# Performance work log

Hardware: AMD Instinct MI355X
Metric: run time of the kernel (lower is better)

Reference implementation:

```python
import jax, jax.numpy as jnp
import numpy as np

N = 100000
E = 1600000
IN_DIM = 128
HID = 64
NUM_CLASSES = 40
K = 3


def setup_inputs() -> dict:
    key = jax.random.key(0)
    ks = jax.random.split(key, 8)
    x = jax.random.normal(ks[0], (N, IN_DIM), dtype=jnp.float32)
    edge_index = jax.random.randint(ks[1], (2, E), 0, N, dtype=jnp.int32)
    s_in = 1.0 / np.sqrt(IN_DIM)
    s_h = 1.0 / np.sqrt(HID)
    W_in = jax.random.uniform(ks[2], (IN_DIM, HID), jnp.float32, -s_in, s_in)
    b_in = jax.random.uniform(ks[3], (HID,), jnp.float32, -s_in, s_in)
    W_layers = jax.random.uniform(ks[4], (K, HID, HID), jnp.float32, -s_h, s_h)
    b_layers = jax.random.uniform(ks[5], (K, HID), jnp.float32, -s_h, s_h)
    W_cls = jax.random.uniform(ks[6], (HID, NUM_CLASSES), jnp.float32, -s_h, s_h)
    b_cls = jax.random.uniform(ks[7], (NUM_CLASSES,), jnp.float32, -s_h, s_h)
    return {"x": x, "edge_index": edge_index, "W_in": W_in, "b_in": b_in,
            "W_layers": W_layers, "b_layers": b_layers, "W_cls": W_cls, "b_cls": b_cls}


def reference(x, edge_index, W_in, b_in, W_layers, b_layers, W_cls, b_cls):
    # eval mode: dropout is identity
    src, dst = edge_index[0], edge_index[1]
    h = jax.nn.relu(x @ W_in + b_in)  # [N, HID]
    for i in range(K):
        # gather messages from src nodes, scatter-add into dst nodes
        agg = jax.ops.segment_sum(h[src], dst, num_segments=N)  # [N, HID]
        h = jax.nn.relu((h + agg) @ W_layers[i] + b_layers[i])
    return h @ W_cls + b_cls  # [N, NUM_CLASSES]
```

## Files before the change

kernel.cpp:

```cpp
#include <hip/hip_runtime.h>
#include <hip/hip_bf16.h>

#define N_NODES 100000
#define E_NUM   1600000
#define IN_DIM  128
#define HID     64
#define NCLS    40
#define NBUCK   782
#define TILE_E  8192
#define NTILE   196
#define BCAP    3072
#define ZROW    N_NODES
#define NTILES_M 6250
#define IN_BLOCKS 1563

typedef __attribute__((ext_vector_type(8))) short bf16x8;
typedef __attribute__((ext_vector_type(4))) float f32x4;

static __device__ __forceinline__ float bflo(unsigned u) {
    return __uint_as_float(u << 16);
}
static __device__ __forceinline__ float bfhi(unsigned u) {
    return __uint_as_float(u & 0xFFFF0000u);
}
static __device__ __forceinline__ unsigned short f2bf(float f) {
    unsigned u = __float_as_uint(f);
    u += 0x7FFFu + ((u >> 16) & 1u);
    return (unsigned short)(u >> 16);
}
static __device__ __forceinline__ unsigned pack2bf(float lo, float hi) {
    return (unsigned)f2bf(lo) | ((unsigned)f2bf(hi) << 16);
}

__global__ void k_prep(const float* __restrict__ Win, const float* __restrict__ Wl,
                       const float* __restrict__ Wc, unsigned* __restrict__ pWin,
                       unsigned* __restrict__ pWl, unsigned* __restrict__ pWc,
                       int* __restrict__ cursor, unsigned short* __restrict__ H0,
                       unsigned short* __restrict__ H1)
{
    const int t = threadIdx.x;
    if (blockIdx.x == 0) {
        for (int i = t; i < NBUCK; i += 256) cursor[i] = 0;
        if (t < 32) {
            ((unsigned*)(H0 + (size_t)ZROW * HID))[t] = 0;
            ((unsigned*)(H1 + (size_t)ZROW * HID))[t] = 0;
        }
    }
    int i = blockIdx.x * 256 + t;
    if (i < 4096) {
        const int nt = i >> 10, ks = (i >> 8) & 3, ln = (i >> 2) & 63, jp = i & 3;
        const int n = nt * 16 + (ln & 15);
        const int k = ks * 32 + (ln >> 4) * 8 + jp * 2;
        pWin[i] = pack2bf(Win[k * HID + n], Win[(k + 1) * HID + n]);
    } else if (i < 10240) {
        int j = i - 4096;
        const int l = j >> 11; j &= 2047;
        const int nt = j >> 9, ks = (j >> 8) & 1, ln = (j >> 2) & 63, jp = j & 3;
        const int n = nt * 16 + (ln & 15);
        const int k = ks * 32 + (ln >> 4) * 8 + jp * 2;
        const float* w = Wl + (size_t)l * HID * HID;
        pWl[i - 4096] = pack2bf(w[k * HID + n], w[(k + 1) * HID + n]);
    } else if (i < 11776) {
        const int j = i - 10240;
        const int nt = j >> 9, ks = (j >> 8) & 1, ln = (j >> 2) & 63, jp = j & 3;
        const int n = nt * 16 + (ln & 15);
        const int k = ks * 32 + (ln >> 4) * 8 + jp * 2;
        pWc[j] = (n < NCLS) ? pack2bf(Wc[k * NCLS + n], Wc[(k + 1) * NCLS + n]) : 0u;
    }
}

__global__ __launch_bounds__(256) void k_build_ingemm(
    const int* __restrict__ ei, int* __restrict__ cursor, int* __restrict__ pairs,
    const float* __restrict__ x, const unsigned* __restrict__ pWin,
    const float* __restrict__ b, unsigned short* __restrict__ H0)
{
    __shared__ int lh[NBUCK];
    __shared__ int lbase[NBUCK];
    __shared__ int lcnt[NBUCK];
    const int t = threadIdx.x;

    if (blockIdx.x < NTILE) {
        for (int i = t; i < NBUCK; i += 256) { lh[i] = 0; lcnt[i] = 0; }
        __syncthreads();
        const int e0 = blockIdx.x * TILE_E;
        for (int k = 0; k < TILE_E; k += 256) {
            int e = e0 + k + t;
            if (e < E_NUM) atomicAdd(&lh[ei[E_NUM + e] >> 7], 1);
        }
        __syncthreads();
        for (int i = t; i < NBUCK; i += 256)
            lbase[i] = lh[i] ? atomicAdd(&cursor[i], lh[i]) : 0;
        __syncthreads();
        for (int k = 0; k < TILE_E; k += 256) {
            int e = e0 + k + t;
            if (e < E_NUM) {
                int src = ei[e];
                int dst = ei[E_NUM + e];
                int bkt = dst >> 7;
                int r   = lbase[bkt] + atomicAdd(&lcnt[bkt], 1);
                if (r < BCAP) pairs[bkt * BCAP + r] = (src << 7) | (dst & 127);
            }
        }
        return;
    }

    const int blk  = blockIdx.x - NTILE;
    const int lane = t & 63;
    const int w    = t >> 6;
    const int tile = blk * 4 + w;
    if (tile >= NTILES_M) return;
    const int quad = lane >> 4;
    const int mrow = lane & 15;
    const int gr   = tile * 16 + mrow;
    const float* xr = x + (size_t)gr * IN_DIM;
    const bf16x8* pb = (const bf16x8*)pWin;

    f32x4 acc0 = {0.f, 0.f, 0.f, 0.f};
    f32x4 acc1 = {0.f, 0.f, 0.f, 0.f};
    f32x4 acc2 = {0.f, 0.f, 0.f, 0.f};
    f32x4 acc3 = {0.f, 0.f, 0.f, 0.f};
    #pragma unroll
    for (int ks = 0; ks < 4; ++ks) {
        const float4 v0 = *(const float4*)(xr + ks * 32 + quad * 8);
        const float4 v1 = *(const float4*)(xr + ks * 32 + quad * 8 + 4);
        union { unsigned u[4]; bf16x8 v; } au;
        au.u[0] = pack2bf(v0.x, v0.y);
        au.u[1] = pack2bf(v0.z, v0.w);
        au.u[2] = pack2bf(v1.x, v1.y);
        au.u[3] = pack2bf(v1.z, v1.w);
        acc0 = __builtin_amdgcn_mfma_f32_16x16x32_bf16(au.v, pb[       ks * 64 + lane], acc0, 0, 0, 0);
        acc1 = __builtin_amdgcn_mfma_f32_16x16x32_bf16(au.v, pb[256 +  ks * 64 + lane], acc1, 0, 0, 0);
        acc2 = __builtin_amdgcn_mfma_f32_16x16x32_bf16(au.v, pb[512 +  ks * 64 + lane], acc2, 0, 0, 0);
        acc3 = __builtin_amdgcn_mfma_f32_16x16x32_bf16(au.v, pb[768 +  ks * 64 + lane], acc3, 0, 0, 0);
    }

    const int colg = lane & 15;
    const int nodeb = tile * 16 + quad * 4;
    const float bv0 = b[     colg];
    const float bv1 = b[16 + colg];
    const float bv2 = b[32 + colg];
    const float bv3 = b[48 + colg];
    #pragma unroll
    for (int r = 0; r < 4; ++r) {
        const size_t ob = (size_t)(nodeb + r) * HID;
        H0[ob      + colg] = f2bf(fmaxf(acc0[r] + bv0, 0.f));
        H0[ob + 16 + colg] = f2bf(fmaxf(acc1[r] + bv1, 0.f));
        H0[ob + 32 + colg] = f2bf(fmaxf(acc2[r] + bv2, 0.f));
        H0[ob + 48 + colg] = f2bf(fmaxf(acc3[r] + bv3, 0.f));
    }
}

__global__ __launch_bounds__(256) void k_bsort(
    const int* __restrict__ cursor, const int* __restrict__ pairs,
    int* __restrict__ srcs, int* __restrict__ row_start, int* __restrict__ row_end)
{
    __shared__ int cnt[128];
    __shared__ int sc[128];
    __shared__ int cur[128];
    const int t = threadIdx.x;
    const int b = blockIdx.x;
    const int beg = b * BCAP;
    const int n_e = min(cursor[b], BCAP);
    if (t < 128) cnt[t] = 0;
    __syncthreads();
    for (int i = t; i < n_e; i += 256)
        atomicAdd(&cnt[pairs[beg + i] & 127], 1);
    __syncthreads();
    if (t < 128) sc[t] = (cnt[t] + 7) & ~7;
    __syncthreads();
    for (int off = 1; off < 128; off <<= 1) {
        int a = (t < 128 && t >= off) ? sc[t - off] : 0;
        __syncthreads();
        if (t < 128) sc[t] += a;
        __syncthreads();
    }
    const int node0 = b << 7;
    if (t < 128) {
        const int pc = (cnt[t] + 7) & ~7;
        const int ex = sc[t] - pc;
        cur[t] = ex;
        const int node = node0 + t;
        if (node < N_NODES) {
            const int rs = beg + ex;
            row_start[node] = rs;
            row_end  [node] = min(rs + pc, beg + BCAP);
        }
        const int fb = beg + ex + cnt[t];
        const int fe = min(beg + ex + pc, beg + BCAP);
        for (int i = fb; i < fe; ++i) srcs[i] = ZROW;
    }
    __syncthreads();
    for (int i = t; i < n_e; i += 256) {
        int p = pairs[beg + i];
        int r = atomicAdd(&cur[p & 127], 1);
        if (r < BCAP) srcs[beg + r] = p >> 7;
    }
}

static __device__ __forceinline__ void gather_tile(
    const int* __restrict__ row_start, const int* __restrict__ row_end,
    const int* __restrict__ srcs, const unsigned short* __restrict__ Hin,
    unsigned (*sup)[36], int row0, int t)
{
    const int lane = t & 63;
    const int w    = t >> 6;
    const int nd   = lane >> 4;
    const int sub  = (lane >> 3) & 1;
    const int fl   = lane & 7;
    const int node = row0 + (w << 2) + nd;

    const int rs = row_start[node];
    int rem = row_end[node] - rs;
    int i = rs + sub;

    float a0 = 0.f, a1 = 0.f, a2 = 0.f, a3 = 0.f;
    float a4 = 0.f, a5 = 0.f, a6 = 0.f, a7 = 0.f;

#define ACC8(u) do { \
        a0 += bflo((u).x); a1 += bfhi((u).x); \
        a2 += bflo((u).y); a3 += bfhi((u).y); \
        a4 += bflo((u).z); a5 += bfhi((u).z); \
        a6 += bflo((u).w); a7 += bfhi((u).w); } while (0)

    while (rem >= 16) {
        const int s0 = srcs[i     ], s1 = srcs[i +  2];
        const int s2 = srcs[i +  4], s3 = srcs[i +  6];
        const int s4 = srcs[i +  8], s5 = srcs[i + 10];
        const int s6 = srcs[i + 12], s7 = srcs[i + 14];
        const uint4 u0 = *(const uint4*)(Hin + (size_t)s0 * HID + 8 * fl);
        const uint4 u1 = *(const uint4*)(Hin + (size_t)s1 * HID + 8 * fl);
        const uint4 u2 = *(const uint4*)(Hin + (size_t)s2 * HID + 8 * fl);
        const uint4 u3 = *(const uint4*)(Hin + (size_t)s3 * HID + 8 * fl);
        const uint4 u4 = *(const uint4*)(Hin + (size_t)s4 * HID + 8 * fl);
        const uint4 u5 = *(const uint4*)(Hin + (size_t)s5 * HID + 8 * fl);
        const uint4 u6 = *(const uint4*)(Hin + (size_t)s6 * HID + 8 * fl);
        const uint4 u7 = *(const uint4*)(Hin + (size_t)s7 * HID + 8 * fl);
        ACC8(u0); ACC8(u1); ACC8(u2); ACC8(u3);
        ACC8(u4); ACC8(u5); ACC8(u6); ACC8(u7);
        i += 16; rem -= 16;
    }
    if (rem >= 8) {
        const int s0 = srcs[i    ], s1 = srcs[i + 2];
        const int s2 = srcs[i + 4], s3 = srcs[i + 6];
        const uint4 u0 = *(const uint4*)(Hin + (size_t)s0 * HID + 8 * fl);
        const uint4 u1 = *(const uint4*)(Hin + (size_t)s1 * HID + 8 * fl);
        const uint4 u2 = *(const uint4*)(Hin + (size_t)s2 * HID + 8 * fl);
        const uint4 u3 = *(const uint4*)(Hin + (size_t)s3 * HID + 8 * fl);
        ACC8(u0); ACC8(u1); ACC8(u2); ACC8(u3);
    }

    a0 += __shfl_xor(a0, 8, 64); a1 += __shfl_xor(a1, 8, 64);
    a2 += __shfl_xor(a2, 8, 64); a3 += __shfl_xor(a3, 8, 64);
    a4 += __shfl_xor(a4, 8, 64); a5 += __shfl_xor(a5, 8, 64);
    a6 += __shfl_xor(a6, 8, 64); a7 += __shfl_xor(a7, 8, 64);

    const uint4 us = *(const uint4*)(Hin + (size_t)node * HID + 8 * fl);
    ACC8(us);
#undef ACC8

    const int r = (w << 2) + nd;
    if (sub == 0) {
        sup[r][4 * fl    ] = pack2bf(a0, a1);
        sup[r][4 * fl + 1] = pack2bf(a2, a3);
    } else {
        sup[r][4 * fl + 2] = pack2bf(a4, a5);
        sup[r][4 * fl + 3] = pack2bf(a6, a7);
    }
}

__global__ __launch_bounds__(256) void k_gather_gemm(
    const int* __restrict__ row_start, const int* __restrict__ row_end,
    const int* __restrict__ srcs,
    const unsigned short* __restrict__ Hin, const unsigned* __restrict__ pWl,
    const float* __restrict__ bl, unsigned short* __restrict__ Hout)
{
    __shared__ unsigned sup[16][36];
    const int t = threadIdx.x;
    const int row0 = blockIdx.x * 16;
    gather_tile(row_start, row_end, srcs, Hin, sup, row0, t);
    __syncthreads();

    const int lane = t & 63;
    const int w    = t >> 6;
    const int quad = lane >> 4;
    const int m    = lane & 15;
    const bf16x8* pb = (const bf16x8*)pWl;
    f32x4 acc = {0.f, 0.f, 0.f, 0.f};
    #pragma unroll
    for (int ks = 0; ks < 2; ++ks) {
        const bf16x8 a  = *(const bf16x8*)&sup[m][ks * 16 + quad * 4];
        const bf16x8 bb = pb[((w << 1) + ks) * 64 + lane];
        acc = __builtin_amdgcn_mfma_f32_16x16x32_bf16(a, bb, acc, 0, 0, 0);
    }
    const int jc = w * 16 + m;
    const float bv = bl[jc];
    #pragma unroll
    for (int r = 0; r < 4; ++r) {
        const int node = row0 + quad * 4 + r;
        Hout[(size_t)node * HID + jc] = f2bf(fmaxf(acc[r] + bv, 0.f));
    }
}

__global__ __launch_bounds__(256) void k_gather_gemm_cls(
    const int* __restrict__ row_start, const int* __restrict__ row_end,
    const int* __restrict__ srcs,
    const unsigned short* __restrict__ Hin, const unsigned* __restrict__ pWl,
    const float* __restrict__ bl, const unsigned* __restrict__ pWc,
    const float* __restrict__ bc, float* __restrict__ out)
{
    __shared__ unsigned sup[16][36];
    __shared__ unsigned short sh2[16][72];
    const int t = threadIdx.x;
    const int row0 = blockIdx.x * 16;
    gather_tile(row_start, row_end, srcs, Hin, sup, row0, t);
    __syncthreads();

    const int lane = t & 63;
    const int w    = t >> 6;
    const int quad = lane >> 4;
    const int m    = lane & 15;
    const bf16x8* pb = (const bf16x8*)pWl;
    f32x4 acc = {0.f, 0.f, 0.f, 0.f};
    #pragma unroll
    for (int ks = 0; ks < 2; ++ks) {
        const bf16x8 a  = *(const bf16x8*)&sup[m][ks * 16 + quad * 4];
        const bf16x8 bb = pb[((w << 1) + ks) * 64 + lane];
        acc = __builtin_amdgcn_mfma_f32_16x16x32_bf16(a, bb, acc, 0, 0, 0);
    }
    const int jc = w * 16 + m;
    const float bv = bl[jc];
    #pragma unroll
    for (int r = 0; r < 4; ++r)
        sh2[quad * 4 + r][jc] = f2bf(fmaxf(acc[r] + bv, 0.f));
    __syncthreads();

    if (w < 3) {
        const bf16x8* pbc = (const bf16x8*)pWc;
        f32x4 c = {0.f, 0.f, 0.f, 0.f};
        #pragma unroll
        for (int ks = 0; ks < 2; ++ks) {
            const bf16x8 a = *(const bf16x8*)&sh2[m][ks * 32 + quad * 8];
            c = __builtin_amdgcn_mfma_f32_16x16x32_bf16(a, pbc[(w * 2 + ks) * 64 + lane], c, 0, 0, 0);
        }
        const int col = w * 16 + m;
        if (col < NCLS) {
            const float bcv = bc[col];
            #pragma unroll
            for (int r = 0; r < 4; ++r)
                out[(size_t)(row0 + quad * 4 + r) * NCLS + col] = c[r] + bcv;
        }
    }
}

extern "C" void kernel_launch(void* const* d_in, const int* in_sizes, int n_in,
                              void* d_out, int out_size, void* d_ws, size_t ws_size,
                              hipStream_t stream)
{
    const float* x        = (const float*)d_in[0];
    const int*   ei       = (const int*)  d_in[1];
    const float* W_in     = (const float*)d_in[2];
    const float* b_in     = (const float*)d_in[3];
    const float* W_layers = (const float*)d_in[4];
    const float* b_layers = (const float*)d_in[5];
    const float* W_cls    = (const float*)d_in[6];
    const float* b_cls    = (const float*)d_in[7];
    float* out = (float*)d_out;

    unsigned short* H0 = (unsigned short*)d_ws;
    unsigned short* H1 = H0 + (size_t)(N_NODES + 1) * HID;
    int* wsp       = (int*)(H1 + (size_t)(N_NODES + 1) * HID);
    int* pairs     = wsp;
    int* srcs      = wsp + NBUCK * BCAP;
    int* row_start = wsp + 2 * NBUCK * BCAP;
    int* row_end   = row_start + 100096;
    int* cursor    = row_end + 100096;
    unsigned* pWin = (unsigned*)(cursor + 1024);
    unsigned* pWl  = pWin + 4096;
    unsigned* pWc  = pWl + 6144;

    const int gemm_blocks = N_NODES / 16;

    k_prep        <<<46, 256, 0, stream>>>(W_in, W_layers, W_cls, pWin, pWl, pWc,
                                           cursor, H0, H1);
    k_build_ingemm<<<NTILE + IN_BLOCKS, 256, 0, stream>>>(ei, cursor, pairs,
                                                          x, pWin, b_in, H0);
    k_bsort       <<<NBUCK, 256, 0, stream>>>(cursor, pairs, srcs, row_start, row_end);

    k_gather_gemm<<<gemm_blocks, 256, 0, stream>>>(
        row_start, row_end, srcs, H0, pWl,          b_layers,        H1);
    k_gather_gemm<<<gemm_blocks, 256, 0, stream>>>(
        row_start, row_end, srcs, H1, pWl + 2048,   b_layers + HID,  H0);
    k_gather_gemm_cls<<<gemm_blocks, 256, 0, stream>>>(
        row_start, row_end, srcs, H0, pWl + 4096,   b_layers + 2*HID,
        pWc, b_cls, out);
}
```

Measured before the change: 255.1 us.

## Build CSR via global per-node degree histogram and direct atomic scatter

Replaces the two-pass bucketed pair sort (local bucket histogram, pairs buffer, per-bucket counting sort) with a per-node degree histogram using global atomics, a per-bucket scan that computes row ranges and per-node cursors, and a direct scatter of source ids into the CSR slots. This removes the intermediate pairs buffer and one full read/write pass over it. In exchange it uses global atomics on 100k counters during both the histogram and the scatter, which may contend, and it adds a memset. Neighbor order within a row becomes nondeterministic, so summation order can vary between runs.

Result: slower. 409.5 us (+60.5%).

```diff
diff --git a/kernel.cpp b/kernel.cpp
--- a/kernel.cpp
+++ b/kernel.cpp
@@ -7,12 +7,15 @@
 #define HID     64
 #define NCLS    40
 #define NBUCK   782
-#define TILE_E  8192
-#define NTILE   196
 #define BCAP    3072
 #define ZROW    N_NODES
 #define NTILES_M 6250
 #define IN_BLOCKS 1563
+#define PREP_BLKS 46
+#define HTILE_E 4096
+#define NHT     392
+#define SC_BLKS 1563
+#define ROWS_BLKS NBUCK
 
 typedef __attribute__((ext_vector_type(8))) short bf16x8;
 typedef __attribute__((ext_vector_type(4))) float f32x4;
@@ -32,19 +35,25 @@
     return (unsigned)f2bf(lo) | ((unsigned)f2bf(hi) << 16);
 }
 
-__global__ void k_prep(const float* __restrict__ Win, const float* __restrict__ Wl,
-                       const float* __restrict__ Wc, unsigned* __restrict__ pWin,
-                       unsigned* __restrict__ pWl, unsigned* __restrict__ pWc,
-                       int* __restrict__ cursor, unsigned short* __restrict__ H0,
-                       unsigned short* __restrict__ H1)
-{
-    const int t = threadIdx.x;
-    if (blockIdx.x == 0) {
-        for (int i = t; i < NBUCK; i += 256) cursor[i] = 0;
-        if (t < 32) {
-            ((unsigned*)(H0 + (size_t)ZROW * HID))[t] = 0;
-            ((unsigned*)(H1 + (size_t)ZROW * HID))[t] = 0;
-        }
+__global__ __launch_bounds__(256) void k_prep_hist(
+    const float* __restrict__ Win, const float* __restrict__ Wl,
+    const float* __restrict__ Wc, unsigned* __restrict__ pWin,
+    unsigned* __restrict__ pWl, unsigned* __restrict__ pWc,
+    unsigned short* __restrict__ H0, unsigned short* __restrict__ H1,
+    const int* __restrict__ ei, int* __restrict__ deg)
+{
+    const int t = threadIdx.x;
+    if (blockIdx.x >= PREP_BLKS) {
+        const int e0 = (blockIdx.x - PREP_BLKS) * HTILE_E;
+        for (int k = 0; k < HTILE_E; k += 256) {
+            const int e = e0 + k + t;
+            if (e < E_NUM) atomicAdd(&deg[ei[E_NUM + e]], 1);
+        }
+        return;
+    }
+    if (blockIdx.x == 0 && t < 32) {
+        ((unsigned*)(H0 + (size_t)ZROW * HID))[t] = 0;
+        ((unsigned*)(H1 + (size_t)ZROW * HID))[t] = 0;
     }
     int i = blockIdx.x * 256 + t;
     if (i < 4096) {
@@ -69,42 +78,51 @@
     }
 }
 
-__global__ __launch_bounds__(256) void k_build_ingemm(
-    const int* __restrict__ ei, int* __restrict__ cursor, int* __restrict__ pairs,
+__global__ __launch_bounds__(256) void k_rows_ingemm(
+    const int* __restrict__ deg, int* __restrict__ cur,
+    int* __restrict__ row_start, int* __restrict__ row_end,
+    int* __restrict__ srcs,
     const float* __restrict__ x, const unsigned* __restrict__ pWin,
     const float* __restrict__ b, unsigned short* __restrict__ H0)
 {
-    __shared__ int lh[NBUCK];
-    __shared__ int lbase[NBUCK];
-    __shared__ int lcnt[NBUCK];
-    const int t = threadIdx.x;
-
-    if (blockIdx.x < NTILE) {
-        for (int i = t; i < NBUCK; i += 256) { lh[i] = 0; lcnt[i] = 0; }
+    __shared__ int sc[128];
+    __shared__ int scnt[128];
+    const int t = threadIdx.x;
+
+    if (blockIdx.x < ROWS_BLKS) {
+        const int bk = blockIdx.x;
+        const int node0 = bk << 7;
+        if (t < 128) {
+            const int c = deg[node0 + t];
+            scnt[t] = c;
+            sc[t] = (c + 7) & ~7;
+        }
         __syncthreads();
-        const int e0 = blockIdx.x * TILE_E;
-        for (int k = 0; k < TILE_E; k += 256) {
-            int e = e0 + k + t;
-            if (e < E_NUM) atomicAdd(&lh[ei[E_NUM + e] >> 7], 1);
-        }
-        __syncthreads();
-        for (int i = t; i < NBUCK; i += 256)
-            lbase[i] = lh[i] ? atomicAdd(&cursor[i], lh[i]) : 0;
-        __syncthreads();
-        for (int k = 0; k < TILE_E; k += 256) {
-            int e = e0 + k + t;
-            if (e < E_NUM) {
-                int src = ei[e];
-                int dst = ei[E_NUM + e];
-                int bkt = dst >> 7;
-                int r   = lbase[bkt] + atomicAdd(&lcnt[bkt], 1);
-                if (r < BCAP) pairs[bkt * BCAP + r] = (src << 7) | (dst & 127);
+        for (int off = 1; off < 128; off <<= 1) {
+            int a = (t < 128 && t >= off) ? sc[t - off] : 0;
+            __syncthreads();
+            if (t < 128) sc[t] += a;
+            __syncthreads();
+        }
+        if (t < 128) {
+            const int cnt = scnt[t];
+            const int pc  = (cnt + 7) & ~7;
+            const int ex  = sc[t] - pc;
+            const int rs  = bk * BCAP + ex;
+            const int bend = (bk + 1) * BCAP;
+            const int re  = min(rs + pc, bend);
+            const int node = node0 + t;
+            if (node < N_NODES) {
+                row_start[node] = rs;
+                row_end[node]   = re;
+                cur[node]       = rs;
             }
+            for (int i = rs + cnt; i < re; ++i) srcs[i] = ZROW;
         }
         return;
     }
 
-    const int blk  = blockIdx.x - NTILE;
+    const int blk  = blockIdx.x - ROWS_BLKS;
     const int lane = t & 63;
     const int w    = t >> 6;
     const int tile = blk * 4 + w;
@@ -150,50 +168,19 @@
     }
 }
 
-__global__ __launch_bounds__(256) void k_bsort(
-    const int* __restrict__ cursor, const int* __restrict__ pairs,
-    int* __restrict__ srcs, int* __restrict__ row_start, int* __restrict__ row_end)
-{
-    __shared__ int cnt[128];
-    __shared__ int sc[128];
-    __shared__ int cur[128];
-    const int t = threadIdx.x;
-    const int b = blockIdx.x;
-    const int beg = b * BCAP;
-    const int n_e = min(cursor[b], BCAP);
-    if (t < 128) cnt[t] = 0;
-    __syncthreads();
-    for (int i = t; i < n_e; i += 256)
-        atomicAdd(&cnt[pairs[beg + i] & 127], 1);
-    __syncthreads();
-    if (t < 128) sc[t] = (cnt[t] + 7) & ~7;
-    __syncthreads();
-    for (int off = 1; off < 128; off <<= 1) {
-        int a = (t < 128 && t >= off) ? sc[t - off] : 0;
-        __syncthreads();
-        if (t < 128) sc[t] += a;
-        __syncthreads();
-    }
-    const int node0 = b << 7;
-    if (t < 128) {
-        const int pc = (cnt[t] + 7) & ~7;
-        const int ex = sc[t] - pc;
-        cur[t] = ex;
-        const int node = node0 + t;
-        if (node < N_NODES) {
-            const int rs = beg + ex;
-            row_start[node] = rs;
-            row_end  [node] = min(rs + pc, beg + BCAP);
-        }
-        const int fb = beg + ex + cnt[t];
-        const int fe = min(beg + ex + pc, beg + BCAP);
-        for (int i = fb; i < fe; ++i) srcs[i] = ZROW;
-    }
-    __syncthreads();
-    for (int i = t; i < n_e; i += 256) {
-        int p = pairs[beg + i];
-        int r = atomicAdd(&cur[p & 127], 1);
-        if (r < BCAP) srcs[beg + r] = p >> 7;
+__global__ __launch_bounds__(256) void k_scatter(
+    const int* __restrict__ ei, int* __restrict__ cur, int* __restrict__ srcs)
+{
+    const int t = threadIdx.x;
+    const int e0 = blockIdx.x * 1024;
+    for (int k = 0; k < 1024; k += 256) {
+        const int e = e0 + k + t;
+        if (e < E_NUM) {
+            const int src = ei[e];
+            const int dst = ei[E_NUM + e];
+            const int slot = atomicAdd(&cur[dst], 1);
+            if (slot < ((dst >> 7) + 1) * BCAP) srcs[slot] = src;
+        }
     }
 }
 
@@ -211,6 +198,7 @@
 
     const int rs = row_start[node];
     int rem = row_end[node] - rs;
+    if (rem < 0) rem = 0;
     int i = rs + sub;
 
     float a0 = 0.f, a1 = 0.f, a2 = 0.f, a3 = 0.f;
@@ -222,7 +210,7 @@
         a4 += bflo((u).z); a5 += bfhi((u).z); \
         a6 += bflo((u).w); a7 += bfhi((u).w); } while (0)
 
-    while (rem >= 16) {
+    for (int nfull = rem >> 4; nfull > 0; --nfull) {
         const int s0 = srcs[i     ], s1 = srcs[i +  2];
         const int s2 = srcs[i +  4], s3 = srcs[i +  6];
         const int s4 = srcs[i +  8], s5 = srcs[i + 10];
@@ -237,9 +225,9 @@
         const uint4 u7 = *(const uint4*)(Hin + (size_t)s7 * HID + 8 * fl);
         ACC8(u0); ACC8(u1); ACC8(u2); ACC8(u3);
         ACC8(u4); ACC8(u5); ACC8(u6); ACC8(u7);
-        i += 16; rem -= 16;
-    }
-    if (rem >= 8) {
+        i += 16;
+    }
+    if (rem & 8) {
         const int s0 = srcs[i    ], s1 = srcs[i + 2];
         const int s2 = srcs[i + 4], s3 = srcs[i + 6];
         const uint4 u0 = *(const uint4*)(Hin + (size_t)s0 * HID + 8 * fl);
@@ -368,24 +356,26 @@
 
     unsigned short* H0 = (unsigned short*)d_ws;
     unsigned short* H1 = H0 + (size_t)(N_NODES + 1) * HID;
-    int* wsp       = (int*)(H1 + (size_t)(N_NODES + 1) * HID);
-    int* pairs     = wsp;
-    int* srcs      = wsp + NBUCK * BCAP;
-    int* row_start = wsp + 2 * NBUCK * BCAP;
+    int* srcs      = (int*)(H1 + (size_t)(N_NODES + 1) * HID);
+    int* row_start = srcs + NBUCK * BCAP;
     int* row_end   = row_start + 100096;
-    int* cursor    = row_end + 100096;
-    unsigned* pWin = (unsigned*)(cursor + 1024);
+    int* deg       = row_end + 100096;
+    int* cur       = deg + 100096;
+    unsigned* pWin = (unsigned*)(cur + 100096);
     unsigned* pWl  = pWin + 4096;
     unsigned* pWc  = pWl + 6144;
 
+    hipMemsetAsync(deg, 0, 100096 * sizeof(int), stream);
+
+    k_prep_hist<<<PREP_BLKS + NHT, 256, 0, stream>>>(
+        W_in, W_layers, W_cls, pWin, pWl, pWc, H0, H1, ei, deg);
+
+    k_rows_ingemm<<<ROWS_BLKS + IN_BLOCKS, 256, 0, stream>>>(
+        deg, cur, row_start, row_end, srcs, x, pWin, b_in, H0);
+
+    k_scatter<<<SC_BLKS, 256, 0, stream>>>(ei, cur, srcs);
+
     const int gemm_blocks = N_NODES / 16;
-
-    k_prep        <<<46, 256, 0, stream>>>(W_in, W_layers, W_cls, pWin, pWl, pWc,
-                                           cursor, H0, H1);
-    k_build_ingemm<<<NTILE + IN_BLOCKS, 256, 0, stream>>>(ei, cursor, pairs,
-                                                          x, pWin, b_in, H0);
-    k_bsort       <<<NBUCK, 256, 0, stream>>>(cursor, pairs, srcs, row_start, row_end);
-
     k_gather_gemm<<<gemm_blocks, 256, 0, stream>>>(
         row_start, row_end, srcs, H0, pWl,          b_layers,        H1);
     k_gather_gemm<<<gemm_blocks, 256, 0, stream>>>(
```

## Regroup preprocessing kernels: fuse partition with weight prep, bucket sort with input GEMM

Applied to the files above, without the earlier changes.

Reshuffles the launch schedule. The edge bucket partition now runs in the same kernel as weight packing, and the per-bucket sort shares a kernel with the input-projection GEMM. The cursor reset moves to a hipMemsetAsync, and the edge and pair loops are unrolled to batch loads ahead of the LDS atomics. In the gather, the self-row load is hoisted before the neighbor loop and the loop count is precomputed. The aim is to cut one dependent kernel launch boundary and raise memory-level parallelism, at the cost of a separate memset launch and more register use.

Result: faster. 233.1 us (-8.6%).

```diff
diff --git a/kernel.cpp b/kernel.cpp
--- a/kernel.cpp
+++ b/kernel.cpp
@@ -13,6 +13,7 @@
 #define ZROW    N_NODES
 #define NTILES_M 6250
 #define IN_BLOCKS 1563
+#define PREP_BLKS 46
 
 typedef __attribute__((ext_vector_type(8))) short bf16x8;
 typedef __attribute__((ext_vector_type(4))) float f32x4;
@@ -32,21 +33,65 @@
     return (unsigned)f2bf(lo) | ((unsigned)f2bf(hi) << 16);
 }
 
-__global__ void k_prep(const float* __restrict__ Win, const float* __restrict__ Wl,
-                       const float* __restrict__ Wc, unsigned* __restrict__ pWin,
-                       unsigned* __restrict__ pWl, unsigned* __restrict__ pWc,
-                       int* __restrict__ cursor, unsigned short* __restrict__ H0,
-                       unsigned short* __restrict__ H1)
-{
+__global__ __launch_bounds__(256) void k_part_prep(
+    const int* __restrict__ ei, int* __restrict__ cursor, int* __restrict__ pairs,
+    const float* __restrict__ Win, const float* __restrict__ Wl,
+    const float* __restrict__ Wc, unsigned* __restrict__ pWin,
+    unsigned* __restrict__ pWl, unsigned* __restrict__ pWc,
+    unsigned short* __restrict__ H0, unsigned short* __restrict__ H1)
+{
+    __shared__ int lh[NBUCK];
+    __shared__ int lbase[NBUCK];
+    __shared__ int lcnt[NBUCK];
     const int t = threadIdx.x;
-    if (blockIdx.x == 0) {
-        for (int i = t; i < NBUCK; i += 256) cursor[i] = 0;
-        if (t < 32) {
-            ((unsigned*)(H0 + (size_t)ZROW * HID))[t] = 0;
-            ((unsigned*)(H1 + (size_t)ZROW * HID))[t] = 0;
-        }
-    }
-    int i = blockIdx.x * 256 + t;
+
+    if (blockIdx.x < NTILE) {
+        for (int i = t; i < NBUCK; i += 256) { lh[i] = 0; lcnt[i] = 0; }
+        __syncthreads();
+        const int e0 = blockIdx.x * TILE_E;
+        #pragma unroll
+        for (int k = 0; k < TILE_E; k += 2048) {
+            int d[8];
+            #pragma unroll
+            for (int j = 0; j < 8; ++j) {
+                const int e = e0 + k + j * 256 + t;
+                d[j] = (e < E_NUM) ? ei[E_NUM + e] : -1;
+            }
+            #pragma unroll
+            for (int j = 0; j < 8; ++j)
+                if (d[j] >= 0) atomicAdd(&lh[d[j] >> 7], 1);
+        }
+        __syncthreads();
+        for (int i = t; i < NBUCK; i += 256)
+            lbase[i] = lh[i] ? atomicAdd(&cursor[i], lh[i]) : 0;
+        __syncthreads();
+        #pragma unroll
+        for (int k = 0; k < TILE_E; k += 1024) {
+            int s[4], d[4];
+            #pragma unroll
+            for (int j = 0; j < 4; ++j) {
+                const int e = e0 + k + j * 256 + t;
+                if (e < E_NUM) { s[j] = ei[e]; d[j] = ei[E_NUM + e]; }
+                else           { s[j] = -1;    d[j] = -1; }
+            }
+            #pragma unroll
+            for (int j = 0; j < 4; ++j) {
+                if (d[j] >= 0) {
+                    const int bkt = d[j] >> 7;
+                    const int r   = lbase[bkt] + atomicAdd(&lcnt[bkt], 1);
+                    if (r < BCAP) pairs[bkt * BCAP + r] = (s[j] << 7) | (d[j] & 127);
+                }
+            }
+        }
+        return;
+    }
+
+    const int bi = blockIdx.x - NTILE;
+    if (bi == 0 && t < 32) {
+        ((unsigned*)(H0 + (size_t)ZROW * HID))[t] = 0;
+        ((unsigned*)(H1 + (size_t)ZROW * HID))[t] = 0;
+    }
+    int i = bi * 256 + t;
     if (i < 4096) {
         const int nt = i >> 10, ks = (i >> 8) & 3, ln = (i >> 2) & 63, jp = i & 3;
         const int n = nt * 16 + (ln & 15);
@@ -69,42 +114,72 @@
     }
 }
 
-__global__ __launch_bounds__(256) void k_build_ingemm(
-    const int* __restrict__ ei, int* __restrict__ cursor, int* __restrict__ pairs,
+__global__ __launch_bounds__(256) void k_bsort_ingemm(
+    const int* __restrict__ cursor, const int* __restrict__ pairs,
+    int* __restrict__ srcs, int* __restrict__ row_start, int* __restrict__ row_end,
     const float* __restrict__ x, const unsigned* __restrict__ pWin,
     const float* __restrict__ b, unsigned short* __restrict__ H0)
 {
-    __shared__ int lh[NBUCK];
-    __shared__ int lbase[NBUCK];
-    __shared__ int lcnt[NBUCK];
+    __shared__ int cnt[128];
+    __shared__ int sc[128];
+    __shared__ int cur[128];
     const int t = threadIdx.x;
 
-    if (blockIdx.x < NTILE) {
-        for (int i = t; i < NBUCK; i += 256) { lh[i] = 0; lcnt[i] = 0; }
-        __syncthreads();
-        const int e0 = blockIdx.x * TILE_E;
-        for (int k = 0; k < TILE_E; k += 256) {
-            int e = e0 + k + t;
-            if (e < E_NUM) atomicAdd(&lh[ei[E_NUM + e] >> 7], 1);
-        }
-        __syncthreads();
-        for (int i = t; i < NBUCK; i += 256)
-            lbase[i] = lh[i] ? atomicAdd(&cursor[i], lh[i]) : 0;
-        __syncthreads();
-        for (int k = 0; k < TILE_E; k += 256) {
-            int e = e0 + k + t;
-            if (e < E_NUM) {
-                int src = ei[e];
-                int dst = ei[E_NUM + e];
-                int bkt = dst >> 7;
-                int r   = lbase[bkt] + atomicAdd(&lcnt[bkt], 1);
-                if (r < BCAP) pairs[bkt * BCAP + r] = (src << 7) | (dst & 127);
+    if (blockIdx.x < NBUCK) {
+        const int bk = blockIdx.x;
+        const int beg = bk * BCAP;
+        const int n_e = min(cursor[bk], BCAP);
+        if (t < 128) cnt[t] = 0;
+        __syncthreads();
+        for (int i = t; i < n_e; i += 1024) {
+            const int p0 = pairs[beg + i];
+            const int p1 = (i + 256 < n_e) ? pairs[beg + i + 256] : -1;
+            const int p2 = (i + 512 < n_e) ? pairs[beg + i + 512] : -1;
+            const int p3 = (i + 768 < n_e) ? pairs[beg + i + 768] : -1;
+            atomicAdd(&cnt[p0 & 127], 1);
+            if (p1 >= 0) atomicAdd(&cnt[p1 & 127], 1);
+            if (p2 >= 0) atomicAdd(&cnt[p2 & 127], 1);
+            if (p3 >= 0) atomicAdd(&cnt[p3 & 127], 1);
+        }
+        __syncthreads();
+        if (t < 128) sc[t] = (cnt[t] + 7) & ~7;
+        __syncthreads();
+        for (int off = 1; off < 128; off <<= 1) {
+            int a = (t < 128 && t >= off) ? sc[t - off] : 0;
+            __syncthreads();
+            if (t < 128) sc[t] += a;
+            __syncthreads();
+        }
+        const int node0 = bk << 7;
+        if (t < 128) {
+            const int pc = (cnt[t] + 7) & ~7;
+            const int ex = sc[t] - pc;
+            cur[t] = ex;
+            const int node = node0 + t;
+            if (node < N_NODES) {
+                const int rs = beg + ex;
+                row_start[node] = rs;
+                row_end  [node] = min(rs + pc, beg + BCAP);
             }
+            const int fb = beg + ex + cnt[t];
+            const int fe = min(beg + ex + pc, beg + BCAP);
+            for (int i = fb; i < fe; ++i) srcs[i] = ZROW;
+        }
+        __syncthreads();
+        for (int i = t; i < n_e; i += 1024) {
+            const int p0 = pairs[beg + i];
+            const int p1 = (i + 256 < n_e) ? pairs[beg + i + 256] : -1;
+            const int p2 = (i + 512 < n_e) ? pairs[beg + i + 512] : -1;
+            const int p3 = (i + 768 < n_e) ? pairs[beg + i + 768] : -1;
+            { const int r = atomicAdd(&cur[p0 & 127], 1); if (r < BCAP) srcs[beg + r] = p0 >> 7; }
+            if (p1 >= 0) { const int r = atomicAdd(&cur[p1 & 127], 1); if (r < BCAP) srcs[beg + r] = p1 >> 7; }
+            if (p2 >= 0) { const int r = atomicAdd(&cur[p2 & 127], 1); if (r < BCAP) srcs[beg + r] = p2 >> 7; }
+            if (p3 >= 0) { const int r = atomicAdd(&cur[p3 & 127], 1); if (r < BCAP) srcs[beg + r] = p3 >> 7; }
         }
         return;
     }
 
-    const int blk  = blockIdx.x - NTILE;
+    const int blk  = blockIdx.x - NBUCK;
     const int lane = t & 63;
     const int w    = t >> 6;
     const int tile = blk * 4 + w;
@@ -150,53 +225,6 @@
     }
 }
 
-__global__ __launch_bounds__(256) void k_bsort(
-    const int* __restrict__ cursor, const int* __restrict__ pairs,
-    int* __restrict__ srcs, int* __restrict__ row_start, int* __restrict__ row_end)
-{
-    __shared__ int cnt[128];
-    __shared__ int sc[128];
-    __shared__ int cur[128];
-    const int t = threadIdx.x;
-    const int b = blockIdx.x;
-    const int beg = b * BCAP;
-    const int n_e = min(cursor[b], BCAP);
-    if (t < 128) cnt[t] = 0;
-    __syncthreads();
-    for (int i = t; i < n_e; i += 256)
-        atomicAdd(&cnt[pairs[beg + i] & 127], 1);
-    __syncthreads();
-    if (t < 128) sc[t] = (cnt[t] + 7) & ~7;
-    __syncthreads();
-    for (int off = 1; off < 128; off <<= 1) {
-        int a = (t < 128 && t >= off) ? sc[t - off] : 0;
-        __syncthreads();
-        if (t < 128) sc[t] += a;
-        __syncthreads();
-    }
-    const int node0 = b << 7;
-    if (t < 128) {
-        const int pc = (cnt[t] + 7) & ~7;
-        const int ex = sc[t] - pc;
-        cur[t] = ex;
-        const int node = node0 + t;
-        if (node < N_NODES) {
-            const int rs = beg + ex;
-            row_start[node] = rs;
-            row_end  [node] = min(rs + pc, beg + BCAP);
-        }
-        const int fb = beg + ex + cnt[t];
-        const int fe = min(beg + ex + pc, beg + BCAP);
-        for (int i = fb; i < fe; ++i) srcs[i] = ZROW;
-    }
-    __syncthreads();
-    for (int i = t; i < n_e; i += 256) {
-        int p = pairs[beg + i];
-        int r = atomicAdd(&cur[p & 127], 1);
-        if (r < BCAP) srcs[beg + r] = p >> 7;
-    }
-}
-
 static __device__ __forceinline__ void gather_tile(
     const int* __restrict__ row_start, const int* __restrict__ row_end,
     const int* __restrict__ srcs, const unsigned short* __restrict__ Hin,
@@ -211,7 +239,10 @@
 
     const int rs = row_start[node];
     int rem = row_end[node] - rs;
+    if (rem < 0) rem = 0;
     int i = rs + sub;
+
+    const uint4 us = *(const uint4*)(Hin + (size_t)node * HID + 8 * fl);
 
     float a0 = 0.f, a1 = 0.f, a2 = 0.f, a3 = 0.f;
     float a4 = 0.f, a5 = 0.f, a6 = 0.f, a7 = 0.f;
@@ -222,7 +253,7 @@
         a4 += bflo((u).z); a5 += bfhi((u).z); \
         a6 += bflo((u).w); a7 += bfhi((u).w); } while (0)
 
-    while (rem >= 16) {
+    for (int nfull = rem >> 4; nfull > 0; --nfull) {
         const int s0 = srcs[i     ], s1 = srcs[i +  2];
         const int s2 = srcs[i +  4], s3 = srcs[i +  6];
         const int s4 = srcs[i +  8], s5 = srcs[i + 10];
@@ -237,9 +268,9 @@
         const uint4 u7 = *(const uint4*)(Hin + (size_t)s7 * HID + 8 * fl);
         ACC8(u0); ACC8(u1); ACC8(u2); ACC8(u3);
         ACC8(u4); ACC8(u5); ACC8(u6); ACC8(u7);
-        i += 16; rem -= 16;
-    }
-    if (rem >= 8) {
+        i += 16;
+    }
+    if (rem & 8) {
         const int s0 = srcs[i    ], s1 = srcs[i + 2];
         const int s2 = srcs[i + 4], s3 = srcs[i + 6];
         const uint4 u0 = *(const uint4*)(Hin + (size_t)s0 * HID + 8 * fl);
@@ -254,7 +285,6 @@
     a4 += __shfl_xor(a4, 8, 64); a5 += __shfl_xor(a5, 8, 64);
     a6 += __shfl_xor(a6, 8, 64); a7 += __shfl_xor(a7, 8, 64);
 
-    const uint4 us = *(const uint4*)(Hin + (size_t)node * HID + 8 * fl);
     ACC8(us);
 #undef ACC8
 
@@ -378,14 +408,15 @@
     unsigned* pWl  = pWin + 4096;
     unsigned* pWc  = pWl + 6144;
 
+    hipMemsetAsync(cursor, 0, 1024 * sizeof(int), stream);
+
+    k_part_prep<<<NTILE + PREP_BLKS, 256, 0, stream>>>(
+        ei, cursor, pairs, W_in, W_layers, W_cls, pWin, pWl, pWc, H0, H1);
+
+    k_bsort_ingemm<<<NBUCK + IN_BLOCKS, 256, 0, stream>>>(
+        cursor, pairs, srcs, row_start, row_end, x, pWin, b_in, H0);
+
     const int gemm_blocks = N_NODES / 16;
-
-    k_prep        <<<46, 256, 0, stream>>>(W_in, W_layers, W_cls, pWin, pWl, pWc,
-                                           cursor, H0, H1);
-    k_build_ingemm<<<NTILE + IN_BLOCKS, 256, 0, stream>>>(ei, cursor, pairs,
-                                                          x, pWin, b_in, H0);
-    k_bsort       <<<NBUCK, 256, 0, stream>>>(cursor, pairs, srcs, row_start, row_end);
-
     k_gather_gemm<<<gemm_blocks, 256, 0, stream>>>(
         row_start, row_end, srcs, H0, pWl,          b_layers,        H1);
     k_gather_gemm<<<gemm_blocks, 256, 0, stream>>>(
```
